# Performance work log

Hardware: AMD Instinct MI355X
Metric: run time of the kernel (lower is better)

Reference implementation:

```python
import jax, jax.numpy as jnp
import numpy as np

N_NODES = 50000
N_EDGES = 800000
IN_CH = 256
OUT_CH = 64
ALPHA = 0.2  # leaky relu slope
NEG_BIG = -9e15


def setup_inputs() -> dict:
    key = jax.random.key(0)
    k1, k2, k3, k4 = jax.random.split(key, 4)
    x = jax.random.normal(k1, (N_NODES, IN_CH), dtype=jnp.float32)
    edge_index = jax.random.randint(k2, (2, N_EDGES), 0, N_NODES, dtype=jnp.int64)
    # xavier-uniform-ish params
    W = jax.random.normal(k3, (IN_CH, OUT_CH), dtype=jnp.float32) * (1.414 * np.sqrt(2.0 / (IN_CH + OUT_CH)))
    a = jax.random.normal(k4, (1, 2 * OUT_CH), dtype=jnp.float32) * (1.414 * np.sqrt(2.0 / (1 + 2 * OUT_CH)))
    return {"x": x, "edge_index": edge_index, "W": W, "a": a}


def reference(x, edge_index, W, a):
    wh = x @ W                                  # [N, F]
    src, dst = edge_index[0], edge_index[1]     # [E], [E]
    F_out = wh.shape[1]
    # (a * [wh_src, wh_dst]).sum(1) == wh_src @ a_src + wh_dst @ a_dst; compute per-node then gather
    e_src = wh @ a[0, :F_out]                   # [N]
    e_dst = wh @ a[0, F_out:]                   # [N]
    e = jax.nn.leaky_relu(e_src[src] + e_dst[dst], ALPHA)[:, None]  # [E, 1]
    e = jnp.where(e > 0, e, jnp.float32(NEG_BIG))
    attention = jax.nn.softmax(e, axis=0)       # global softmax over ALL edges (faithful to source)
    msgs = attention * wh[src]                  # [E, F]
    h_prime = jax.ops.segment_sum(msgs, dst, num_segments=wh.shape[0])  # [N, F]
    return jax.nn.elu(h_prime)
```

## Files before the change

### kernel.cpp

```cpp
#include <hip/hip_runtime.h>
#include <hip/hip_bf16.h>

#define N_NODES 50000
#define N_EDGES 800000
#define IN_CH 256
#define OUT_CH 64
#define M_CONST 12.0f
#define NBLK_E 3125
#define NBLK_N 196

typedef __bf16 bfvec8 __attribute__((ext_vector_type(8)));
typedef float floatx4 __attribute__((ext_vector_type(4)));
typedef int intx4 __attribute__((ext_vector_type(4)));

#define WS_WHB   0
#define WS_W32   6400000
#define WS_PSRC  9600000
#define WS_SRC16 11200000
#define WS_DST16 12800000
#define WS_RANK  14400000
#define WS_CNT   16000000
#define WS_ROWP  16200000
#define WS_WTH   16400000
#define WS_WTL   16433024
#define WS_ESRC  16465920
#define WS_EDST  16665920
#define WS_BTOT  16865920
#define WS_ZS    16866432

__device__ __forceinline__ float loadf(const void* p, size_t i, int isf32) {
    return isf32 ? ((const float*)p)[i]
                 : __bfloat162float(((const __hip_bfloat16*)p)[i]);
}
__device__ __forceinline__ void load_edge(const int* __restrict__ ei, int i, int f64,
                                          int& s, int& d) {
    if (f64) {
        int2 ps = ((const int2*)ei)[i];
        int2 pd = ((const int2*)ei)[N_EDGES + i];
        s = ps.x; d = pd.x;
    } else {
        s = ei[i]; d = ei[N_EDGES + i];
    }
    s = min(max(s, 0), N_NODES - 1);
    d = min(max(d, 0), N_NODES - 1);
}

__device__ __forceinline__ int detect_isf(const unsigned* __restrict__ xw, int tid) {
    unsigned lo = xw[tid] & 0xFFFFu;
    unsigned e8 = (lo >> 7) & 0xFFu;
    return (__syncthreads_count((int)(e8 >= 96u && e8 <= 144u)) < 192) ? 1 : 0;
}

__global__ __launch_bounds__(256) void k_prep(const void* __restrict__ Wv,
                                              const unsigned* __restrict__ xw,
                                              __bf16* __restrict__ Wth,
                                              __bf16* __restrict__ Wtl,
                                              int* __restrict__ cnt,
                                              float* __restrict__ Zs) {
    int tid = threadIdx.x;
    int isf = detect_isf(xw, tid);
    int t = blockIdx.x * 256 + tid;
    int c = t >> 8, k = t & 255;
    float w = loadf(Wv, (size_t)k * OUT_CH + c, isf);
    __bf16 h = (__bf16)w;
    Wth[t] = h;
    Wtl[t] = (__bf16)(w - (float)h);
    if (t < N_NODES / 4) ((intx4*)cnt)[t] = (intx4){0, 0, 0, 0};
    if (t < 512) ((intx4*)Zs)[t] = (intx4){0, 0, 0, 0};
}

__global__ __launch_bounds__(256, 2) void k_mm(const void* __restrict__ xv,
                                               const __bf16* __restrict__ Wth,
                                               const __bf16* __restrict__ Wtl,
                                               const void* __restrict__ av,
                                               __bf16* __restrict__ whb,
                                               float* __restrict__ esrc,
                                               float* __restrict__ edst) {
    __shared__ __bf16 lW[2][64 * 256];
    int tid = threadIdx.x;
    int isf = detect_isf((const unsigned*)xv, tid);
    int gw = (blockIdx.x * 256 + tid) >> 6;
    int lane = tid & 63;
    int m = lane & 15, quad = lane >> 4;
    int nb = gw * 16;
    bool active = gw < N_NODES / 16;

    floatx4 x0[8], x1[8];
    bfvec8 xa[8];
    if (active) {
        if (isf) {
            const float* xr = (const float*)xv + (size_t)(nb + m) * IN_CH + quad * 8;
#pragma unroll
            for (int s = 0; s < 8; ++s) {
                x0[s] = *(const floatx4*)(xr + s * 32);
                x1[s] = *(const floatx4*)(xr + s * 32 + 4);
            }
        } else {
            const __bf16* xr = (const __bf16*)xv + (size_t)(nb + m) * IN_CH + quad * 8;
#pragma unroll
            for (int s = 0; s < 8; ++s) xa[s] = *(const bfvec8*)(xr + s * 32);
        }
    }

#pragma unroll
    for (int i = 0; i < 8; ++i) {
        int f = i * 256 + tid;
        int r = f >> 5, c = f & 31;
        int cs = c ^ (r & 31);
        *(bfvec8*)(&lW[0][r * 256 + cs * 8]) = *(const bfvec8*)(Wth + r * 256 + c * 8);
        *(bfvec8*)(&lW[1][r * 256 + cs * 8]) = *(const bfvec8*)(Wtl + r * 256 + c * 8);
    }
    __syncthreads();

    if (!active) return;

    floatx4 acc[4];
#pragma unroll
    for (int ct = 0; ct < 4; ++ct) acc[ct] = (floatx4){0.f, 0.f, 0.f, 0.f};

    if (isf) {
#pragma unroll
        for (int s = 0; s < 8; ++s) {
            float v[8];
            *(floatx4*)(v)     = x0[s];
            *(floatx4*)(v + 4) = x1[s];
            bfvec8 ahi, alo;
#pragma unroll
            for (int j = 0; j < 8; ++j) {
                __bf16 h = (__bf16)v[j];
                ahi[j] = h;
                alo[j] = (__bf16)(v[j] - (float)h);
            }
#pragma unroll
            for (int ct = 0; ct < 4; ++ct) {
                int row = ct * 16 + m;
                int cs = ((s * 4 + quad) ^ (row & 31)) * 8;
                bfvec8 bhi = *(const bfvec8*)(&lW[0][row * 256 + cs]);
                bfvec8 blo = *(const bfvec8*)(&lW[1][row * 256 + cs]);
                acc[ct] = __builtin_amdgcn_mfma_f32_16x16x32_bf16(ahi, blo, acc[ct], 0, 0, 0);
                acc[ct] = __builtin_amdgcn_mfma_f32_16x16x32_bf16(alo, bhi, acc[ct], 0, 0, 0);
                acc[ct] = __builtin_amdgcn_mfma_f32_16x16x32_bf16(ahi, bhi, acc[ct], 0, 0, 0);
            }
        }
    } else {
#pragma unroll
        for (int s = 0; s < 8; ++s) {
#pragma unroll
            for (int ct = 0; ct < 4; ++ct) {
                int row = ct * 16 + m;
                int cs = ((s * 4 + quad) ^ (row & 31)) * 8;
                bfvec8 bhi = *(const bfvec8*)(&lW[0][row * 256 + cs]);
                bfvec8 blo = *(const bfvec8*)(&lW[1][row * 256 + cs]);
                acc[ct] = __builtin_amdgcn_mfma_f32_16x16x32_bf16(xa[s], blo, acc[ct], 0, 0, 0);
                acc[ct] = __builtin_amdgcn_mfma_f32_16x16x32_bf16(xa[s], bhi, acc[ct], 0, 0, 0);
            }
        }
    }

    float a1[4], a2[4];
#pragma unroll
    for (int ct = 0; ct < 4; ++ct) {
        a1[ct] = loadf(av, ct * 16 + m, isf);
        a2[ct] = loadf(av, OUT_CH + ct * 16 + m, isf);
    }
#pragma unroll
    for (int r = 0; r < 4; ++r) {
        int node = nb + quad * 4 + r;
        float s1 = 0.f, s2 = 0.f;
#pragma unroll
        for (int ct = 0; ct < 4; ++ct) {
            float vv = acc[ct][r];
            whb[(size_t)node * OUT_CH + ct * 16 + m] = (__bf16)vv;
            s1 += vv * a1[ct];
            s2 += vv * a2[ct];
        }
#pragma unroll
        for (int off = 1; off < 16; off <<= 1) {
            s1 += __shfl_xor(s1, off);
            s2 += __shfl_xor(s2, off);
        }
        if (m == 0) { esrc[node] = s1; edst[node] = s2; }
    }
}

__global__ __launch_bounds__(256) void k_edge(const int* __restrict__ ei,
                                              const float* __restrict__ esrc,
                                              const float* __restrict__ edst,
                                              unsigned short* __restrict__ src16,
                                              unsigned short* __restrict__ dst16,
                                              unsigned short* __restrict__ rank16,
                                              int* __restrict__ cnt) {
    int t = threadIdx.x;
    int f64 = (__syncthreads_or(ei[2 * t + 1]) == 0) ? 1 : 0;
    int i = blockIdx.x * 256 + t;
    int s, d;
    load_edge(ei, i, f64, s, d);
    src16[i] = (unsigned short)s;
    dst16[i] = (unsigned short)d;
    float v = esrc[s] + edst[d];
    if (v > 0.0f) {
        int r = atomicAdd(&cnt[d], 1);
        rank16[i] = (unsigned short)r;
    }
}

__global__ __launch_bounds__(256) void k_scanA(const int* __restrict__ cnt,
                                               int* __restrict__ rowptr,
                                               int* __restrict__ btot) {
    int t = threadIdx.x, lane = t & 63, wid = t >> 6;
    int idx = blockIdx.x * 256 + t;
    int v = (idx < N_NODES) ? cnt[idx] : 0;
    int incl = v;
#pragma unroll
    for (int off = 1; off < 64; off <<= 1) {
        int u = __shfl_up(incl, off);
        if (lane >= off) incl += u;
    }
    __shared__ int wsum[4];
    if (lane == 63) wsum[wid] = incl;
    __syncthreads();
    int wbase = 0;
#pragma unroll
    for (int w = 0; w < 4; ++w) if (w < wid) wbase += wsum[w];
    if (idx < N_NODES) rowptr[idx] = wbase + incl - v;
    if (t == 255) btot[blockIdx.x] = wbase + incl;
}

__global__ __launch_bounds__(256) void k_scanBC(const int* __restrict__ btot,
                                                int* __restrict__ rowptr) {
    int b = blockIdx.x, t = threadIdx.x;
    int v = (t < b) ? btot[t] : 0;
#pragma unroll
    for (int off = 32; off > 0; off >>= 1) v += __shfl_down(v, off);
    __shared__ int sm[4];
    if ((t & 63) == 0) sm[t >> 6] = v;
    __syncthreads();
    int base = sm[0] + sm[1] + sm[2] + sm[3];
    int idx = b * 256 + t;
    if (idx < N_NODES) rowptr[idx] += base;
}

__global__ __launch_bounds__(256) void k_exp(const float* __restrict__ esrc,
                                             const float* __restrict__ edst,
                                             const unsigned short* __restrict__ src16,
                                             const unsigned short* __restrict__ dst16,
                                             const unsigned short* __restrict__ rank16,
                                             const int* __restrict__ rowptr,
                                             float* __restrict__ w32,
                                             unsigned short* __restrict__ psrc,
                                             float* __restrict__ Zs) {
    int i = blockIdx.x * 256 + threadIdx.x;
    int s = src16[i], d = dst16[i];
    float v = esrc[s] + edst[d];
    float t = (v > 0.0f) ? expf(v - M_CONST) : 0.0f;
    if (v > 0.0f) {
        int pos = rowptr[d] + rank16[i];
        w32[pos] = t;
        psrc[pos] = (unsigned short)s;
    }
#pragma unroll
    for (int off = 32; off > 0; off >>= 1) t += __shfl_down(t, off);
    __shared__ float sm[4];
    if ((threadIdx.x & 63) == 0) sm[threadIdx.x >> 6] = t;
    __syncthreads();
    if (threadIdx.x == 0)
        atomicAdd(&Zs[(blockIdx.x & 63) * 32], sm[0] + sm[1] + sm[2] + sm[3]);
}

__global__ __launch_bounds__(256) void k_gather(const int* __restrict__ rowptr,
                                                const int* __restrict__ cnt,
                                                const float* __restrict__ w32,
                                                const unsigned short* __restrict__ psrc,
                                                const __bf16* __restrict__ whb,
                                                const float* __restrict__ Zs,
                                                float* __restrict__ out) {
    int gw = (blockIdx.x * 256 + (int)threadIdx.x) >> 6;
    int lane = threadIdx.x & 63;
    int sub = lane >> 3;
    int cg  = lane & 7;
    int beg = rowptr[gw];
    int end = beg + cnt[gw];

    float z = Zs[lane * 32];
#pragma unroll
    for (int off = 32; off > 0; off >>= 1) z += __shfl_xor(z, off);
    float invZ = (z > 0.0f) ? 1.0f / z : 0.0f;

    float acc[8];
#pragma unroll
    for (int k = 0; k < 8; ++k) acc[k] = 0.0f;

    for (int j0 = beg; j0 < end; j0 += 8) {
        int j = j0 + sub;
        bool valid = j < end;
        int jj = valid ? j : beg;
        float t = valid ? w32[jj] : 0.0f;
        int s = psrc[jj];
        bfvec8 v = *(const bfvec8*)(whb + (size_t)s * OUT_CH + cg * 8);
#pragma unroll
        for (int k = 0; k < 8; ++k) acc[k] += t * (float)v[k];
    }

#pragma unroll
    for (int mask = 8; mask <= 32; mask <<= 1) {
#pragma unroll
        for (int k = 0; k < 8; ++k) acc[k] += __shfl_xor(acc[k], mask);
    }

    if (sub == 0) {
        floatx4 o0, o1;
#pragma unroll
        for (int k = 0; k < 4; ++k) {
            float h = acc[k] * invZ;
            o0[k] = h > 0.0f ? h : expf(h) - 1.0f;
        }
#pragma unroll
        for (int k = 0; k < 4; ++k) {
            float h = acc[4 + k] * invZ;
            o1[k] = h > 0.0f ? h : expf(h) - 1.0f;
        }
        float* dst = out + (size_t)gw * OUT_CH + cg * 8;
        *(floatx4*)(dst)     = o0;
        *(floatx4*)(dst + 4) = o1;
    }
}

extern "C" void kernel_launch(void* const* d_in, const int* in_sizes, int n_in,
                              void* d_out, int out_size, void* d_ws, size_t ws_size,
                              hipStream_t stream) {
    const void* x  = d_in[0];
    const int* ei  = (const int*)d_in[1];
    const void* W  = d_in[2];
    const void* a  = d_in[3];
    float* out     = (float*)d_out;

    char* ws = (char*)d_ws;
    __bf16* whb  = (__bf16*)(ws + WS_WHB);
    float* w32   = (float*)(ws + WS_W32);
    unsigned short* psrc   = (unsigned short*)(ws + WS_PSRC);
    unsigned short* src16  = (unsigned short*)(ws + WS_SRC16);
    unsigned short* dst16  = (unsigned short*)(ws + WS_DST16);
    unsigned short* rank16 = (unsigned short*)(ws + WS_RANK);
    int* cnt     = (int*)(ws + WS_CNT);
    int* rowptr  = (int*)(ws + WS_ROWP);
    __bf16* Wth  = (__bf16*)(ws + WS_WTH);
    __bf16* Wtl  = (__bf16*)(ws + WS_WTL);
    float* esrc  = (float*)(ws + WS_ESRC);
    float* edst  = (float*)(ws + WS_EDST);
    int*   btot  = (int*)(ws + WS_BTOT);
    float* Zs    = (float*)(ws + WS_ZS);

    k_prep  <<<64,        256, 0, stream>>>(W, (const unsigned*)x, Wth, Wtl, cnt, Zs);
    k_mm    <<<782,       256, 0, stream>>>(x, Wth, Wtl, a, whb, esrc, edst);
    k_edge  <<<NBLK_E,    256, 0, stream>>>(ei, esrc, edst, src16, dst16, rank16, cnt);
    k_scanA <<<NBLK_N,    256, 0, stream>>>(cnt, rowptr, btot);
    k_scanBC<<<NBLK_N,    256, 0, stream>>>(btot, rowptr);
    k_exp   <<<NBLK_E,    256, 0, stream>>>(esrc, edst, src16, dst16, rank16, rowptr, w32, psrc, Zs);
    k_gather<<<N_NODES/4, 256, 0, stream>>>(rowptr, cnt, w32, psrc, whb, Zs, out);
}
```

Baseline: 173.0 us.

## Fuse exp/Z into edge pass, merge scans, recompute weights in gather

```diff
diff --git a/kernel.cpp b/kernel.cpp
--- a/kernel.cpp
+++ b/kernel.cpp
@@ -14,7 +14,6 @@
 typedef int intx4 __attribute__((ext_vector_type(4)));
 
 #define WS_WHB   0
-#define WS_W32   6400000
 #define WS_PSRC  9600000
 #define WS_SRC16 11200000
 #define WS_DST16 12800000
@@ -25,7 +24,6 @@
 #define WS_WTL   16433024
 #define WS_ESRC  16465920
 #define WS_EDST  16665920
-#define WS_BTOT  16865920
 #define WS_ZS    16866432
 
 __device__ __forceinline__ float loadf(const void* p, size_t i, int isf32) {
@@ -189,7 +187,8 @@
                                               unsigned short* __restrict__ src16,
                                               unsigned short* __restrict__ dst16,
                                               unsigned short* __restrict__ rank16,
-                                              int* __restrict__ cnt) {
+                                              int* __restrict__ cnt,
+                                              float* __restrict__ Zs) {
     int t = threadIdx.x;
     int f64 = (__syncthreads_or(ei[2 * t + 1]) == 0) ? 1 : 0;
     int i = blockIdx.x * 256 + t;
@@ -198,17 +197,32 @@
     src16[i] = (unsigned short)s;
     dst16[i] = (unsigned short)d;
     float v = esrc[s] + edst[d];
+    unsigned short r = 0xFFFFu;
+    float tt = 0.0f;
     if (v > 0.0f) {
-        int r = atomicAdd(&cnt[d], 1);
-        rank16[i] = (unsigned short)r;
-    }
-}
-
-__global__ __launch_bounds__(256) void k_scanA(const int* __restrict__ cnt,
-                                               int* __restrict__ rowptr,
-                                               int* __restrict__ btot) {
-    int t = threadIdx.x, lane = t & 63, wid = t >> 6;
-    int idx = blockIdx.x * 256 + t;
+        r = (unsigned short)atomicAdd(&cnt[d], 1);
+        tt = expf(v - M_CONST);
+    }
+    rank16[i] = r;
+#pragma unroll
+    for (int off = 32; off > 0; off >>= 1) tt += __shfl_down(tt, off);
+    __shared__ float sm[4];
+    if ((t & 63) == 0) sm[t >> 6] = tt;
+    __syncthreads();
+    if (t == 0)
+        atomicAdd(&Zs[(blockIdx.x & 63) * 32], sm[0] + sm[1] + sm[2] + sm[3]);
+}
+
+__global__ __launch_bounds__(256) void k_scan(const int* __restrict__ cnt,
+                                              int* __restrict__ rowptr) {
+    int b = blockIdx.x, t = threadIdx.x, lane = t & 63, wid = t >> 6;
+    int base = 0;
+    for (int i = t; i < b * 256; i += 256) base += cnt[i];
+#pragma unroll
+    for (int off = 32; off > 0; off >>= 1) base += __shfl_down(base, off);
+    __shared__ int sb[4];
+    if (lane == 0) sb[wid] = base;
+    int idx = b * 256 + t;
     int v = (idx < N_NODES) ? cnt[idx] : 0;
     int incl = v;
 #pragma unroll
@@ -219,57 +233,27 @@
     __shared__ int wsum[4];
     if (lane == 63) wsum[wid] = incl;
     __syncthreads();
-    int wbase = 0;
+    int wbase = sb[0] + sb[1] + sb[2] + sb[3];
 #pragma unroll
     for (int w = 0; w < 4; ++w) if (w < wid) wbase += wsum[w];
     if (idx < N_NODES) rowptr[idx] = wbase + incl - v;
-    if (t == 255) btot[blockIdx.x] = wbase + incl;
-}
-
-__global__ __launch_bounds__(256) void k_scanBC(const int* __restrict__ btot,
-                                                int* __restrict__ rowptr) {
-    int b = blockIdx.x, t = threadIdx.x;
-    int v = (t < b) ? btot[t] : 0;
-#pragma unroll
-    for (int off = 32; off > 0; off >>= 1) v += __shfl_down(v, off);
-    __shared__ int sm[4];
-    if ((t & 63) == 0) sm[t >> 6] = v;
-    __syncthreads();
-    int base = sm[0] + sm[1] + sm[2] + sm[3];
-    int idx = b * 256 + t;
-    if (idx < N_NODES) rowptr[idx] += base;
-}
-
-__global__ __launch_bounds__(256) void k_exp(const float* __restrict__ esrc,
-                                             const float* __restrict__ edst,
-                                             const unsigned short* __restrict__ src16,
-                                             const unsigned short* __restrict__ dst16,
-                                             const unsigned short* __restrict__ rank16,
-                                             const int* __restrict__ rowptr,
-                                             float* __restrict__ w32,
-                                             unsigned short* __restrict__ psrc,
-                                             float* __restrict__ Zs) {
+}
+
+__global__ __launch_bounds__(256) void k_place(const unsigned short* __restrict__ src16,
+                                               const unsigned short* __restrict__ dst16,
+                                               const unsigned short* __restrict__ rank16,
+                                               const int* __restrict__ rowptr,
+                                               unsigned short* __restrict__ psrc) {
     int i = blockIdx.x * 256 + threadIdx.x;
-    int s = src16[i], d = dst16[i];
-    float v = esrc[s] + edst[d];
-    float t = (v > 0.0f) ? expf(v - M_CONST) : 0.0f;
-    if (v > 0.0f) {
-        int pos = rowptr[d] + rank16[i];
-        w32[pos] = t;
-        psrc[pos] = (unsigned short)s;
-    }
-#pragma unroll
-    for (int off = 32; off > 0; off >>= 1) t += __shfl_down(t, off);
-    __shared__ float sm[4];
-    if ((threadIdx.x & 63) == 0) sm[threadIdx.x >> 6] = t;
-    __syncthreads();
-    if (threadIdx.x == 0)
-        atomicAdd(&Zs[(blockIdx.x & 63) * 32], sm[0] + sm[1] + sm[2] + sm[3]);
+    unsigned short r = rank16[i];
+    if (r != 0xFFFFu)
+        psrc[rowptr[dst16[i]] + r] = src16[i];
 }
 
 __global__ __launch_bounds__(256) void k_gather(const int* __restrict__ rowptr,
                                                 const int* __restrict__ cnt,
-                                                const float* __restrict__ w32,
+                                                const float* __restrict__ esrc,
+                                                const float* __restrict__ edst,
                                                 const unsigned short* __restrict__ psrc,
                                                 const __bf16* __restrict__ whb,
                                                 const float* __restrict__ Zs,
@@ -280,6 +264,7 @@
     int cg  = lane & 7;
     int beg = rowptr[gw];
     int end = beg + cnt[gw];
+    float edst_d = edst[gw];
 
     float z = Zs[lane * 32];
 #pragma unroll
@@ -294,8 +279,8 @@
         int j = j0 + sub;
         bool valid = j < end;
         int jj = valid ? j : beg;
-        float t = valid ? w32[jj] : 0.0f;
         int s = psrc[jj];
+        float t = valid ? expf(esrc[s] + edst_d - M_CONST) : 0.0f;
         bfvec8 v = *(const bfvec8*)(whb + (size_t)s * OUT_CH + cg * 8);
 #pragma unroll
         for (int k = 0; k < 8; ++k) acc[k] += t * (float)v[k];
@@ -336,7 +321,6 @@
 
     char* ws = (char*)d_ws;
     __bf16* whb  = (__bf16*)(ws + WS_WHB);
-    float* w32   = (float*)(ws + WS_W32);
     unsigned short* psrc   = (unsigned short*)(ws + WS_PSRC);
     unsigned short* src16  = (unsigned short*)(ws + WS_SRC16);
     unsigned short* dst16  = (unsigned short*)(ws + WS_DST16);
@@ -347,14 +331,12 @@
     __bf16* Wtl  = (__bf16*)(ws + WS_WTL);
     float* esrc  = (float*)(ws + WS_ESRC);
     float* edst  = (float*)(ws + WS_EDST);
-    int*   btot  = (int*)(ws + WS_BTOT);
     float* Zs    = (float*)(ws + WS_ZS);
 
     k_prep  <<<64,        256, 0, stream>>>(W, (const unsigned*)x, Wth, Wtl, cnt, Zs);
     k_mm    <<<782,       256, 0, stream>>>(x, Wth, Wtl, a, whb, esrc, edst);
-    k_edge  <<<NBLK_E,    256, 0, stream>>>(ei, esrc, edst, src16, dst16, rank16, cnt);
-    k_scanA <<<NBLK_N,    256, 0, stream>>>(cnt, rowptr, btot);
-    k_scanBC<<<NBLK_N,    256, 0, stream>>>(btot, rowptr);
-    k_exp   <<<NBLK_E,    256, 0, stream>>>(esrc, edst, src16, dst16, rank16, rowptr, w32, psrc, Zs);
-    k_gather<<<N_NODES/4, 256, 0, stream>>>(rowptr, cnt, w32, psrc, whb, Zs, out);
-}
+    k_edge  <<<NBLK_E,    256, 0, stream>>>(ei, esrc, edst, src16, dst16, rank16, cnt, Zs);
+    k_scan  <<<NBLK_N,    256, 0, stream>>>(cnt, rowptr);
+    k_place <<<NBLK_E,    256, 0, stream>>>(src16, dst16, rank16, rowptr, psrc);
+    k_gather<<<N_NODES/4, 256, 0, stream>>>(rowptr, cnt, esrc, edst, psrc, whb, Zs, out);
+}
```

Result: slower. 189.5 us (+9.5%).
